# Kernel tuning notes

Measured on AMD Instinct MI355X. Metric: run time of the kernel, lower is better.

The kernel has to match this reference:

```python
import jax, jax.numpy as jnp
import numpy as np

LAMB = 0.05
ITERS = 3
EPS = 1e-6


def _l2norm(x):
    return x / jnp.linalg.norm(x, axis=-1, keepdims=True)


def setup_inputs() -> dict:
    key = jax.random.key(0)
    k1, k2, k3, k4 = jax.random.split(key, 4)
    Bi, Bt, R, W, D = 128, 128, 36, 50, 1024
    # region / word features, L2-normalized so fg_sims are cosine similarities
    imgs = _l2norm(jax.random.normal(k1, (Bi, R, D), dtype=jnp.float32))
    caps = _l2norm(jax.random.normal(k2, (Bt, W, D), dtype=jnp.float32))
    # valid lengths; force max so static shapes R, W match int(lens.max())
    img_lens = jax.random.randint(k3, (Bi,), 10, R + 1).astype(jnp.int32)
    img_lens = img_lens.at[0].set(R)
    cap_lens = jax.random.randint(k4, (Bt,), 5, W + 1).astype(jnp.int32)
    cap_lens = cap_lens.at[0].set(W)
    return {"imgs": imgs, "caps": caps, "img_lens": img_lens, "cap_lens": cap_lens}


def _forward(imgs, caps, img_lens, cap_lens):
    Bi, R, D = imgs.shape
    Bt, W, _ = caps.shape
    # fine-grained similarities: [Bi, Bt, R, W]
    fg_sims = jnp.einsum('ird,cwd->icrw', imgs, caps)
    # fine-grained validity mask from lengths
    img_m = (jnp.arange(R)[None, :] < img_lens[:, None])          # [Bi, R]
    cap_m = (jnp.arange(W)[None, :] < cap_lens[:, None])          # [Bt, W]
    mask = (img_m[:, None, :, None] & cap_m[None, :, None, :])    # [Bi, Bt, R, W] bool
    maskf = mask.astype(fg_sims.dtype)

    # _ave_init: uniform marginals over valid rows / cols
    rmask = img_m[:, None, :].astype(fg_sims.dtype) * jnp.ones((1, Bt, 1), fg_sims.dtype)
    r = rmask / rmask.sum(axis=-1, keepdims=True)                 # [Bi, Bt, R]
    cmask = cap_m[None, :, :].astype(fg_sims.dtype) * jnp.ones((Bi, 1, 1), fg_sims.dtype)
    c = cmask / cmask.sum(axis=-1, keepdims=True)                 # [Bi, Bt, W]

    # Sinkhorn-Knopp on cost (1 - fg_sims), masked entries get cost +inf -> P=0
    P = jnp.where(mask, jnp.exp(-(1.0 - fg_sims) / LAMB), 0.0)
    P = P / (P.sum(axis=(-2, -1), keepdims=True) + EPS)
    for _ in range(ITERS):
        u = P.sum(axis=-1) + EPS                                  # [Bi, Bt, R]
        P = P * (r / u)[..., None]
        v = P.sum(axis=-2) + EPS                                  # [Bi, Bt, W]
        P = P * (c / v)[..., None, :]

    sims = (fg_sims * P * maskf).sum(axis=(-2, -1))               # [Bi, Bt]
    return sims


def reference(imgs, caps, img_lens, cap_lens):
    return _forward(imgs, caps, img_lens, cap_lens)
```

## Files before the change

kernel.cpp:

```cpp
#include <hip/hip_runtime.h>
#include <stdint.h>

#define BI 128
#define BT 128
#define RR 36
#define WW 50
#define DD 1024
#define NN 6400
#define SEPS 1e-6f
#define L2E20 28.853900817779268f

typedef __attribute__((ext_vector_type(8))) short short8v;
typedef __attribute__((ext_vector_type(4))) float float4v;
typedef __attribute__((ext_vector_type(2))) unsigned int uint2v;

__device__ __forceinline__ unsigned short f2bf(float f){
  unsigned u = __float_as_uint(f);
  return (unsigned short)((u + 0x7FFFu + ((u >> 16) & 1u)) >> 16);
}

__global__ __launch_bounds__(256) void prefix_kernel(
    const int* __restrict__ il, const int* __restrict__ cl,
    int* __restrict__ rowoff, int* __restrict__ coloff){
  __shared__ int buf[2][128];
  const int t = threadIdx.x;
  const int which = t >> 7, j = t & 127;
  const int v = which ? cl[j] : il[j];
  buf[which][j] = v;
  __syncthreads();
  #pragma unroll
  for (int off = 1; off < 128; off <<= 1){
    int x = (j >= off) ? buf[which][j - off] : 0;
    __syncthreads();
    buf[which][j] += x;
    __syncthreads();
  }
  int* dst = which ? coloff : rowoff;
  dst[j] = buf[which][j] - v;
  if (j == 127) dst[128] = buf[which][127];
}

__global__ __launch_bounds__(256) void gather_cvt_kernel(
    const float* __restrict__ imgs, const float* __restrict__ caps,
    const int* __restrict__ il, const int* __restrict__ cl,
    const int* __restrict__ rowoff, const int* __restrict__ coloff,
    unsigned short* __restrict__ Ab, unsigned short* __restrict__ Bb){
  const int b = blockIdx.x;
  const int t = threadIdx.x;
  if (b < BI * RR){
    const int i = b / RR, r = b % RR;
    if (r >= il[i]) return;
    const float4 v = *(const float4*)(imgs + (size_t)b * DD + t * 4);
    ushort4 o = make_ushort4(f2bf(v.x), f2bf(v.y), f2bf(v.z), f2bf(v.w));
    *(ushort4*)(Ab + (size_t)(rowoff[i] + r) * DD + t * 4) = o;
  } else {
    const int bb = b - BI * RR;
    const int c = bb / WW, w = bb % WW;
    if (w >= cl[c]) return;
    const float4 v = *(const float4*)(caps + (size_t)bb * DD + t * 4);
    ushort4 o = make_ushort4(f2bf(v.x), f2bf(v.y), f2bf(v.z), f2bf(v.w));
    *(ushort4*)(Bb + (size_t)(coloff[c] + w) * DD + t * 4) = o;
  }
}

__global__ __launch_bounds__(256) void gemm_kernel(
    const unsigned short* __restrict__ A, const unsigned short* __restrict__ B,
    const int* __restrict__ rowoff, const int* __restrict__ coloff,
    float* __restrict__ C){
  __shared__ __align__(16) unsigned char LDS[36864];
  const int Mp = rowoff[BI];
  const int Np = coloff[BT];
  const int nnb = (Np + 63) >> 6;
  const int nact = ((Mp + 127) >> 7) * nnb;
  const int bx = blockIdx.x;
  if (bx >= nact) return;
  const int mb = bx / nnb, nb = bx - mb * nnb;
  const int m0 = mb * 128, n0 = nb * 64;

  const int tid = threadIdx.x;
  const int lane = tid & 63, wv = tid >> 6;
  const int l15 = lane & 15, lhi = lane >> 4;
  const int wr = wv >> 1, wc = wv & 1;

  const unsigned short* sp[3];
  #pragma unroll
  for (int j = 0; j < 3; j++){
    const int u = j * 256 + tid;
    const int v = (u < 512) ? u : (u - 512);
    const int sup = v >> 3, slot = v & 7;
    const int sub = slot ^ (sup & 7);
    const int row = sup * 2 + (sub >> 2);
    const int kg  = sub & 3;
    sp[j] = ((u < 512) ? (A + (size_t)(m0 + row) * DD)
                       : (B + (size_t)(n0 + row) * DD)) + kg * 8;
  }

  float4v acc[4][2];
  #pragma unroll
  for (int a1 = 0; a1 < 4; a1++)
    #pragma unroll
    for (int b1 = 0; b1 < 2; b1++)
      acc[a1][b1] = (float4v){0.f, 0.f, 0.f, 0.f};

#define STAGE(BUF, CH) { \
    _Pragma("unroll") \
    for (int j = 0; j < 3; j++) \
      __builtin_amdgcn_global_load_lds( \
          (const __attribute__((address_space(1))) void*)(sp[j] + (CH) * 32), \
          (__attribute__((address_space(3))) void*)(LDS + (BUF) * 12288 + (j * 256 + tid) * 16), \
          16, 0, 0); }

#define LUNIT(row) (((row) >> 1) * 8 + (((((row) & 1) << 2) + lhi) ^ (((row) >> 1) & 7)))

#define COMPUTE(BUF) { \
    short8v af[4], bf[2]; \
    _Pragma("unroll") \
    for (int tr = 0; tr < 4; tr++){ \
      const int row = wr * 64 + tr * 16 + l15; \
      af[tr] = *(const short8v*)(LDS + (BUF) * 12288 + LUNIT(row) * 16); \
    } \
    _Pragma("unroll") \
    for (int tw = 0; tw < 2; tw++){ \
      const int row = wc * 32 + tw * 16 + l15; \
      bf[tw] = *(const short8v*)(LDS + (BUF) * 12288 + 8192 + LUNIT(row) * 16); \
    } \
    _Pragma("unroll") \
    for (int tr = 0; tr < 4; tr++) \
      _Pragma("unroll") \
      for (int tw = 0; tw < 2; tw++) \
        acc[tr][tw] = __builtin_amdgcn_mfma_f32_16x16x32_bf16( \
            af[tr], bf[tw], acc[tr][tw], 0, 0, 0); }

#define WAIT6  asm volatile("s_waitcnt vmcnt(6)" ::: "memory")
#define WAIT3  asm volatile("s_waitcnt vmcnt(3)" ::: "memory")
#define WAIT0  asm volatile("s_waitcnt vmcnt(0)" ::: "memory")
#define BAR    __builtin_amdgcn_s_barrier()

  STAGE(0, 0);
  STAGE(1, 1);
  #pragma unroll 1
  for (int k = 0; k < 10; k++){
    const int c = 3 * k;
    STAGE(2, c + 2); WAIT6; BAR; COMPUTE(0); BAR;
    STAGE(0, c + 3); WAIT6; BAR; COMPUTE(1); BAR;
    STAGE(1, c + 4); WAIT6; BAR; COMPUTE(2); BAR;
  }
  WAIT3; BAR; COMPUTE(0); BAR;
  WAIT0; BAR; COMPUTE(1);

#undef STAGE
#undef LUNIT
#undef COMPUTE
#undef WAIT6
#undef WAIT3
#undef WAIT0
#undef BAR

  #pragma unroll
  for (int tr = 0; tr < 4; tr++)
    #pragma unroll
    for (int tw = 0; tw < 2; tw++)
      #pragma unroll
      for (int j = 0; j < 4; j++){
        int m = m0 + wr * 64 + tr * 16 + lhi * 4 + j;
        int n = n0 + wc * 32 + tw * 16 + l15;
        __builtin_nontemporal_store(acc[tr][tw][j], &C[(size_t)m * NN + n]);
      }
}

template<int CTRL>
__device__ __forceinline__ float dpp_add(float x){
  int y = __builtin_amdgcn_mov_dpp(__float_as_int(x), CTRL, 0xF, 0xF, true);
  return x + __int_as_float(y);
}
__device__ __forceinline__ float q16sum(float x){
  x = dpp_add<0x121>(x);
  x = dpp_add<0x122>(x);
  x = dpp_add<0x124>(x);
  x = dpp_add<0x128>(x);
  return x;
}
__device__ __forceinline__ float pl16comb(float x){
  unsigned xi = __float_as_uint(x);
  uint2v r = __builtin_amdgcn_permlane16_swap(xi, xi, false, false);
  return __uint_as_float(r[0]) + __uint_as_float(r[1]);
}
__device__ __forceinline__ float pl32comb(float x){
  unsigned xi = __float_as_uint(x);
  uint2v r = __builtin_amdgcn_permlane32_swap(xi, xi, false, false);
  return __uint_as_float(r[0]) + __uint_as_float(r[1]);
}

__global__ __launch_bounds__(256) void sink_kernel(
    const float* __restrict__ fg, const int* __restrict__ il,
    const int* __restrict__ cl, const int* __restrict__ rowoff,
    const int* __restrict__ coloff, float* __restrict__ out){
  const int lane = threadIdx.x & 63;
  const int gw = blockIdx.x * 4 + (threadIdx.x >> 6);
  const int i = gw >> 7, c = gw & 127;
  const int q = lane >> 4, t = lane & 15;

  const int ilen = __builtin_amdgcn_readfirstlane(il[i]);
  const int clen = __builtin_amdgcn_readfirstlane(cl[c]);
  const int ro   = __builtin_amdgcn_readfirstlane(rowoff[i]);
  const int co   = __builtin_amdgcn_readfirstlane(coloff[c]);
  const float* base = fg + (size_t)ro * NN + co;
  const float inv_il = __fdividef(1.0f, (float)ilen);
  const float inv_cl = __fdividef(1.0f, (float)clen);
  const bool v0 = (t      < clen);
  const bool v1 = (t + 16 < clen);
  const bool v2 = (t + 32 < clen);
  const bool v3 = (t + 48 < clen);
  const int r0 = 9 * q;
  const int off0 = r0 * NN + t;

  float p0[9], p1[9], p2[9], p3[9];
  float ts = 0.f;
  #pragma unroll
  for (int k = 0; k < 9; k++){
    const bool rv = (r0 + k) < ilen;
    const float a0 = base[off0 + k * NN];
    const float a1 = base[off0 + k * NN + 16];
    const float a2 = base[off0 + k * NN + 32];
    const float a3 = base[off0 + k * NN + 48];
    p0[k] = (rv && v0) ? exp2f(fmaf(a0, L2E20, -L2E20)) : 0.f;
    p1[k] = (rv && v1) ? exp2f(fmaf(a1, L2E20, -L2E20)) : 0.f;
    p2[k] = (rv && v2) ? exp2f(fmaf(a2, L2E20, -L2E20)) : 0.f;
    p3[k] = (rv && v3) ? exp2f(fmaf(a3, L2E20, -L2E20)) : 0.f;
    ts += (p0[k] + p1[k]) + (p2[k] + p3[k]);
  }
  ts = q16sum(ts);
  ts = pl16comb(ts);
  ts = pl32comb(ts);
  const float sc = __fdividef(1.0f, ts + SEPS);
  #pragma unroll
  for (int k = 0; k < 9; k++){
    p0[k] *= sc; p1[k] *= sc; p2[k] *= sc; p3[k] *= sc;
  }

  for (int it = 0; it < 3; it++){
    #pragma unroll
    for (int k = 0; k < 9; k++){
      float u = (p0[k] + p1[k]) + (p2[k] + p3[k]);
      u = q16sum(u);
      const float rs = __fdividef(inv_il, u + SEPS);
      p0[k] *= rs; p1[k] *= rs; p2[k] *= rs; p3[k] *= rs;
    }
    float s0 = 0.f, s1 = 0.f, s2 = 0.f, s3 = 0.f;
    #pragma unroll
    for (int k = 0; k < 9; k++){
      s0 += p0[k]; s1 += p1[k]; s2 += p2[k]; s3 += p3[k];
    }
    s0 = pl16comb(s0); s0 = pl32comb(s0);
    s1 = pl16comb(s1); s1 = pl32comb(s1);
    s2 = pl16comb(s2); s2 = pl32comb(s2);
    s3 = pl16comb(s3); s3 = pl32comb(s3);
    const float cs0 = __fdividef(inv_cl, s0 + SEPS);
    const float cs1 = __fdividef(inv_cl, s1 + SEPS);
    const float cs2 = __fdividef(inv_cl, s2 + SEPS);
    const float cs3 = __fdividef(inv_cl, s3 + SEPS);
    #pragma unroll
    for (int k = 0; k < 9; k++){
      p0[k] *= cs0; p1[k] *= cs1; p2[k] *= cs2; p3[k] *= cs3;
    }
  }

  float sim = 0.f;
  #pragma unroll
  for (int k = 0; k < 9; k++){
    sim = fmaf(base[off0 + k * NN],      p0[k], sim);
    sim = fmaf(base[off0 + k * NN + 16], p1[k], sim);
    sim = fmaf(base[off0 + k * NN + 32], p2[k], sim);
    sim = fmaf(base[off0 + k * NN + 48], p3[k], sim);
  }
  sim = q16sum(sim);
  sim = pl16comb(sim);
  sim = pl32comb(sim);
  if (lane == 0) out[i * BT + c] = sim;
}

extern "C" void kernel_launch(void* const* d_in, const int* in_sizes, int n_in,
                              void* d_out, int out_size, void* d_ws, size_t ws_size,
                              hipStream_t stream){
  const float* imgs = (const float*)d_in[0];
  const float* caps = (const float*)d_in[1];
  const int* il = (const int*)d_in[2];
  const int* cl = (const int*)d_in[3];
  float* out = (float*)d_out;

  unsigned short* Ab = (unsigned short*)d_ws;
  unsigned short* Bb = Ab + (size_t)BI * RR * DD;
  float* fg = (float*)(Bb + (size_t)BT * WW * DD);
  int* rowoff = (int*)(fg + (size_t)BI * RR * NN);
  int* coloff = rowoff + 129;

  prefix_kernel<<<1, 256, 0, stream>>>(il, cl, rowoff, coloff);
  gather_cvt_kernel<<<BI * RR + BT * WW, 256, 0, stream>>>(
      imgs, caps, il, cl, rowoff, coloff, Ab, Bb);
  gemm_kernel<<<36 * 100, 256, 0, stream>>>(Ab, Bb, rowoff, coloff, fg);
  sink_kernel<<<(BI * BT) / 4, 256, 0, stream>>>(fg, il, cl, rowoff, coloff, out);
}
```

Before: 113.0 us.

## Drop prefix kernel via in-wave length sums and widen GEMM N-tile to 128

Removes the separate prefix-scan launch. Each consumer kernel now computes its row and column offsets with a masked wave-wide DPP/permlane reduction over the length arrays. The GEMM output tile grows from 128x64 to 128x128, so each wave does 4x4 MFMAs, LDS rises to 48KB, and half as many blocks are launched. This saves one launch and improves operand reuse, at the cost of redundant per-block reductions, more registers and LDS, and lower occupancy.

```diff
diff --git a/kernel.cpp b/kernel.cpp
--- a/kernel.cpp
+++ b/kernel.cpp
@@ -19,74 +19,83 @@
   return (unsigned short)((u + 0x7FFFu + ((u >> 16) & 1u)) >> 16);
 }
 
-__global__ __launch_bounds__(256) void prefix_kernel(
-    const int* __restrict__ il, const int* __restrict__ cl,
-    int* __restrict__ rowoff, int* __restrict__ coloff){
-  __shared__ int buf[2][128];
-  const int t = threadIdx.x;
-  const int which = t >> 7, j = t & 127;
-  const int v = which ? cl[j] : il[j];
-  buf[which][j] = v;
-  __syncthreads();
-  #pragma unroll
-  for (int off = 1; off < 128; off <<= 1){
-    int x = (j >= off) ? buf[which][j - off] : 0;
-    __syncthreads();
-    buf[which][j] += x;
-    __syncthreads();
-  }
-  int* dst = which ? coloff : rowoff;
-  dst[j] = buf[which][j] - v;
-  if (j == 127) dst[128] = buf[which][127];
+template<int CTRL>
+__device__ __forceinline__ int dpp_addi(int x){
+  int y = __builtin_amdgcn_mov_dpp(x, CTRL, 0xF, 0xF, true);
+  return x + y;
+}
+__device__ __forceinline__ int iwaveSum(int x){
+  x = dpp_addi<0x121>(x);
+  x = dpp_addi<0x122>(x);
+  x = dpp_addi<0x124>(x);
+  x = dpp_addi<0x128>(x);
+  {
+    uint2v r = __builtin_amdgcn_permlane16_swap((unsigned)x, (unsigned)x, false, false);
+    x = (int)r[0] + (int)r[1];
+  }
+  {
+    uint2v r = __builtin_amdgcn_permlane32_swap((unsigned)x, (unsigned)x, false, false);
+    x = (int)r[0] + (int)r[1];
+  }
+  return x;
+}
+__device__ __forceinline__ int maskedSum128(const int* __restrict__ v,
+                                            int lim, int lane){
+  const int a = v[2 * lane];
+  const int b = v[2 * lane + 1];
+  int s = ((2 * lane) < lim ? a : 0) + ((2 * lane + 1) < lim ? b : 0);
+  return iwaveSum(s);
 }
 
 __global__ __launch_bounds__(256) void gather_cvt_kernel(
     const float* __restrict__ imgs, const float* __restrict__ caps,
     const int* __restrict__ il, const int* __restrict__ cl,
-    const int* __restrict__ rowoff, const int* __restrict__ coloff,
     unsigned short* __restrict__ Ab, unsigned short* __restrict__ Bb){
   const int b = blockIdx.x;
   const int t = threadIdx.x;
+  const int lane = t & 63;
   if (b < BI * RR){
     const int i = b / RR, r = b % RR;
     if (r >= il[i]) return;
+    const int ro = maskedSum128(il, i, lane);
     const float4 v = *(const float4*)(imgs + (size_t)b * DD + t * 4);
     ushort4 o = make_ushort4(f2bf(v.x), f2bf(v.y), f2bf(v.z), f2bf(v.w));
-    *(ushort4*)(Ab + (size_t)(rowoff[i] + r) * DD + t * 4) = o;
+    *(ushort4*)(Ab + (size_t)(ro + r) * DD + t * 4) = o;
   } else {
     const int bb = b - BI * RR;
     const int c = bb / WW, w = bb % WW;
     if (w >= cl[c]) return;
+    const int co = maskedSum128(cl, c, lane);
     const float4 v = *(const float4*)(caps + (size_t)bb * DD + t * 4);
     ushort4 o = make_ushort4(f2bf(v.x), f2bf(v.y), f2bf(v.z), f2bf(v.w));
-    *(ushort4*)(Bb + (size_t)(coloff[c] + w) * DD + t * 4) = o;
+    *(ushort4*)(Bb + (size_t)(co + w) * DD + t * 4) = o;
   }
 }
 
 __global__ __launch_bounds__(256) void gemm_kernel(
     const unsigned short* __restrict__ A, const unsigned short* __restrict__ B,
-    const int* __restrict__ rowoff, const int* __restrict__ coloff,
+    const int* __restrict__ il, const int* __restrict__ cl,
     float* __restrict__ C){
-  __shared__ __align__(16) unsigned char LDS[36864];
-  const int Mp = rowoff[BI];
-  const int Np = coloff[BT];
-  const int nnb = (Np + 63) >> 6;
+  __shared__ __align__(16) unsigned char LDS[49152];
+  const int tid = threadIdx.x;
+  const int lane = tid & 63, wv = tid >> 6;
+  const int Mp = __builtin_amdgcn_readfirstlane(maskedSum128(il, BI, lane));
+  const int Np = __builtin_amdgcn_readfirstlane(maskedSum128(cl, BT, lane));
+  const int nnb = (Np + 127) >> 7;
   const int nact = ((Mp + 127) >> 7) * nnb;
   const int bx = blockIdx.x;
   if (bx >= nact) return;
   const int mb = bx / nnb, nb = bx - mb * nnb;
-  const int m0 = mb * 128, n0 = nb * 64;
-
-  const int tid = threadIdx.x;
-  const int lane = tid & 63, wv = tid >> 6;
+  const int m0 = mb * 128, n0 = nb * 128;
+
   const int l15 = lane & 15, lhi = lane >> 4;
   const int wr = wv >> 1, wc = wv & 1;
 
-  const unsigned short* sp[3];
-  #pragma unroll
-  for (int j = 0; j < 3; j++){
+  const unsigned short* sp[4];
+  #pragma unroll
+  for (int j = 0; j < 4; j++){
     const int u = j * 256 + tid;
-    const int v = (u < 512) ? u : (u - 512);
+    const int v = u & 511;
     const int sup = v >> 3, slot = v & 7;
     const int sub = slot ^ (sup & 7);
     const int row = sup * 2 + (sub >> 2);
@@ -95,44 +104,44 @@
                        : (B + (size_t)(n0 + row) * DD)) + kg * 8;
   }
 
-  float4v acc[4][2];
+  float4v acc[4][4];
   #pragma unroll
   for (int a1 = 0; a1 < 4; a1++)
     #pragma unroll
-    for (int b1 = 0; b1 < 2; b1++)
+    for (int b1 = 0; b1 < 4; b1++)
       acc[a1][b1] = (float4v){0.f, 0.f, 0.f, 0.f};
 
 #define STAGE(BUF, CH) { \
     _Pragma("unroll") \
-    for (int j = 0; j < 3; j++) \
+    for (int j = 0; j < 4; j++) \
       __builtin_amdgcn_global_load_lds( \
           (const __attribute__((address_space(1))) void*)(sp[j] + (CH) * 32), \
-          (__attribute__((address_space(3))) void*)(LDS + (BUF) * 12288 + (j * 256 + tid) * 16), \
+          (__attribute__((address_space(3))) void*)(LDS + (BUF) * 16384 + (j * 256 + tid) * 16), \
           16, 0, 0); }
 
 #define LUNIT(row) (((row) >> 1) * 8 + (((((row) & 1) << 2) + lhi) ^ (((row) >> 1) & 7)))
 
 #define COMPUTE(BUF) { \
-    short8v af[4], bf[2]; \
+    short8v af[4], bf[4]; \
     _Pragma("unroll") \
     for (int tr = 0; tr < 4; tr++){ \
       const int row = wr * 64 + tr * 16 + l15; \
-      af[tr] = *(const short8v*)(LDS + (BUF) * 12288 + LUNIT(row) * 16); \
+      af[tr] = *(const short8v*)(LDS + (BUF) * 16384 + LUNIT(row) * 16); \
     } \
     _Pragma("unroll") \
-    for (int tw = 0; tw < 2; tw++){ \
-      const int row = wc * 32 + tw * 16 + l15; \
-      bf[tw] = *(const short8v*)(LDS + (BUF) * 12288 + 8192 + LUNIT(row) * 16); \
+    for (int tw = 0; tw < 4; tw++){ \
+      const int row = wc * 64 + tw * 16 + l15; \
+      bf[tw] = *(const short8v*)(LDS + (BUF) * 16384 + 8192 + LUNIT(row) * 16); \
     } \
     _Pragma("unroll") \
     for (int tr = 0; tr < 4; tr++) \
       _Pragma("unroll") \
-      for (int tw = 0; tw < 2; tw++) \
+      for (int tw = 0; tw < 4; tw++) \
         acc[tr][tw] = __builtin_amdgcn_mfma_f32_16x16x32_bf16( \
             af[tr], bf[tw], acc[tr][tw], 0, 0, 0); }
 
-#define WAIT6  asm volatile("s_waitcnt vmcnt(6)" ::: "memory")
-#define WAIT3  asm volatile("s_waitcnt vmcnt(3)" ::: "memory")
+#define WAIT8  asm volatile("s_waitcnt vmcnt(8)" ::: "memory")
+#define WAIT4  asm volatile("s_waitcnt vmcnt(4)" ::: "memory")
 #define WAIT0  asm volatile("s_waitcnt vmcnt(0)" ::: "memory")
 #define BAR    __builtin_amdgcn_s_barrier()
 
@@ -141,29 +150,29 @@
   #pragma unroll 1
   for (int k = 0; k < 10; k++){
     const int c = 3 * k;
-    STAGE(2, c + 2); WAIT6; BAR; COMPUTE(0); BAR;
-    STAGE(0, c + 3); WAIT6; BAR; COMPUTE(1); BAR;
-    STAGE(1, c + 4); WAIT6; BAR; COMPUTE(2); BAR;
-  }
-  WAIT3; BAR; COMPUTE(0); BAR;
+    STAGE(2, c + 2); WAIT8; BAR; COMPUTE(0); BAR;
+    STAGE(0, c + 3); WAIT8; BAR; COMPUTE(1); BAR;
+    STAGE(1, c + 4); WAIT8; BAR; COMPUTE(2); BAR;
+  }
+  WAIT4; BAR; COMPUTE(0); BAR;
   WAIT0; BAR; COMPUTE(1);
 
 #undef STAGE
 #undef LUNIT
 #undef COMPUTE
-#undef WAIT6
-#undef WAIT3
+#undef WAIT8
+#undef WAIT4
 #undef WAIT0
 #undef BAR
 
   #pragma unroll
   for (int tr = 0; tr < 4; tr++)
     #pragma unroll
-    for (int tw = 0; tw < 2; tw++)
+    for (int tw = 0; tw < 4; tw++)
       #pragma unroll
       for (int j = 0; j < 4; j++){
         int m = m0 + wr * 64 + tr * 16 + lhi * 4 + j;
-        int n = n0 + wc * 32 + tw * 16 + l15;
+        int n = n0 + wc * 64 + tw * 16 + l15;
         __builtin_nontemporal_store(acc[tr][tw][j], &C[(size_t)m * NN + n]);
       }
 }
@@ -193,8 +202,7 @@
 
 __global__ __launch_bounds__(256) void sink_kernel(
     const float* __restrict__ fg, const int* __restrict__ il,
-    const int* __restrict__ cl, const int* __restrict__ rowoff,
-    const int* __restrict__ coloff, float* __restrict__ out){
+    const int* __restrict__ cl, float* __restrict__ out){
   const int lane = threadIdx.x & 63;
   const int gw = blockIdx.x * 4 + (threadIdx.x >> 6);
   const int i = gw >> 7, c = gw & 127;
@@ -202,8 +210,8 @@
 
   const int ilen = __builtin_amdgcn_readfirstlane(il[i]);
   const int clen = __builtin_amdgcn_readfirstlane(cl[c]);
-  const int ro   = __builtin_amdgcn_readfirstlane(rowoff[i]);
-  const int co   = __builtin_amdgcn_readfirstlane(coloff[c]);
+  const int ro   = __builtin_amdgcn_readfirstlane(maskedSum128(il, i, lane));
+  const int co   = __builtin_amdgcn_readfirstlane(maskedSum128(cl, c, lane));
   const float* base = fg + (size_t)ro * NN + co;
   const float inv_il = __fdividef(1.0f, (float)ilen);
   const float inv_cl = __fdividef(1.0f, (float)clen);
@@ -291,12 +299,9 @@
   unsigned short* Ab = (unsigned short*)d_ws;
   unsigned short* Bb = Ab + (size_t)BI * RR * DD;
   float* fg = (float*)(Bb + (size_t)BT * WW * DD);
-  int* rowoff = (int*)(fg + (size_t)BI * RR * NN);
-  int* coloff = rowoff + 129;
-
-  prefix_kernel<<<1, 256, 0, stream>>>(il, cl, rowoff, coloff);
+
   gather_cvt_kernel<<<BI * RR + BT * WW, 256, 0, stream>>>(
-      imgs, caps, il, cl, rowoff, coloff, Ab, Bb);
-  gemm_kernel<<<36 * 100, 256, 0, stream>>>(Ab, Bb, rowoff, coloff, fg);
-  sink_kernel<<<(BI * BT) / 4, 256, 0, stream>>>(fg, il, cl, rowoff, coloff, out);
-}
+      imgs, caps, il, cl, Ab, Bb);
+  gemm_kernel<<<36 * 50, 256, 0, stream>>>(Ab, Bb, il, cl, fg);
+  sink_kernel<<<(BI * BT) / 4, 256, 0, stream>>>(fg, il, cl, out);
+}
```

Measured after the change: 105.7 us. -6.5%, faster.
